# Kernel optimization log

Hardware: AMD Instinct MI355X
Metric: run time of the kernel (lower is better)

The kernel has to match this reference:

```python
import jax, jax.numpy as jnp
import numpy as np
from jax import lax

# Parameter physical bounds, order: smax, k1, k2, kb
MIN_BOUNDS = np.array([10.0, 0.01, 0.001, 0.001], dtype=np.float32)
MAX_BOUNDS = np.array([500.0, 0.9, 0.2, 0.1], dtype=np.float32)

T, B, H = 2048, 32, 64
N_FORCING, N_STATE, N_PARAM, N_FLUX = 2, 2, 4, 4


def setup_inputs() -> dict:
    key = jax.random.key(0)
    k1, k2 = jax.random.split(key)
    # forcings: [T, B, H, 2] -> (P precip, PET potential ET), non-negative
    forcings = jax.random.uniform(k1, (T, B, H, N_FORCING), dtype=jnp.float32)
    # initial states: [B, H, 2], model default is zeros
    states = jnp.zeros((B, H, N_STATE), dtype=jnp.float32)
    # unconstrained params in [0,1): [B, H, 4] (static -> repeated over T)
    parameters = jax.random.uniform(k2, (B, H, N_PARAM), dtype=jnp.float32)
    return {"forcings": forcings, "states": states, "parameters": parameters}


def _core(states_t, forcings_t, params_t):
    # states_t: [B,H,2], forcings_t: [B,H,2], params_t: [B,H,4]
    S1, S2 = states_t[..., 0], states_t[..., 1]
    P, PET = forcings_t[..., 0], forcings_t[..., 1]
    smax, k1, k2, kb = (params_t[..., i] for i in range(4))
    # flux_calculator
    et = PET * jnp.clip(S1 / smax, 0.0, 1.0)
    q1 = k1 * S1
    perc = k2 * S1
    qb = kb * S2
    fluxes = jnp.stack([et, q1, perc, qb], axis=-1)  # [B,H,4]
    # state_updater (mass balance), then clamp_(min=0)
    S1n = S1 + P - et - q1 - perc
    S2n = S2 + perc - qb
    new_states = jnp.maximum(jnp.stack([S1n, S2n], axis=-1), 0.0)  # [B,H,2]
    return fluxes, new_states


def reference(forcings, states, parameters):
    # transform parameters to physical bounds: min + (max-min)*u
    min_b = jnp.asarray(MIN_BOUNDS)
    max_b = jnp.asarray(MAX_BOUNDS)
    phys_params = min_b + (max_b - min_b) * parameters  # [B,H,4] (static)

    def step(carry, f_t):
        fluxes_t, new_states = _core(carry, f_t, phys_params)
        return new_states, (fluxes_t, new_states)

    _, (fluxes_seq, states_seq) = lax.scan(step, states, forcings)
    # fluxes_seq: [T,B,H,4], states_seq: [T,B,H,2]
    return fluxes_seq, states_seq
```

## Files before the change

kernel.cpp:

```cpp
#include <hip/hip_runtime.h>
#include <stdint.h>

#define T_STEPS 2048
#define N_CELLS 2048
#define GCELLS  64
#define NGROUPS (N_CELLS / GCELLS)
#define TS      128
#define NTILES  (T_STEPS / TS)
#define BCHUNK  16
#define NCHUNK  (T_STEPS / BCHUNK)
#define FLUX_ELEMS ((size_t)T_STEPS * N_CELLS * 4)

#define AS3 __attribute__((address_space(3)))
#define AS1 __attribute__((address_space(1)))

__device__ __forceinline__ void step_state(float& S1, float& S2,
                                           float P, float PET,
                                           float inv_smax, float a, float b,
                                           float k2) {
    float ratio = fminf(S1 * inv_smax, 1.0f);
    float u1    = fmaf(S1, a, P);
    float S1n   = fmaxf(fmaf(-PET, ratio, u1), 0.0f);
    float perc  = k2 * S1;
    float S2n   = fmaxf(fmaf(S2, b, perc), 0.0f);
    S1 = S1n; S2 = S2n;
}

__global__ void __launch_bounds__(64) hydro_scan(
    const float* __restrict__ forc,
    const float* __restrict__ init_state,
    const float* __restrict__ params,
    float* __restrict__ out)
{
    __shared__ float4 tile[2][TS * 32];

    const int g    = blockIdx.x;
    const int L    = threadIdx.x;
    const int cell = g * GCELLS + L;

    float2* out_s = (float2*)(out + FLUX_ELEMS);

    const float4* gf4 = (const float4*)forc;
    const size_t lane_off = (size_t)(L >> 5) * 1024 + (size_t)g * 32 + (L & 31);

    const float4 u = ((const float4*)params)[cell];
    float2 s0 = ((const float2*)init_state)[cell];

    {
        const float4* gp = gf4 + lane_off;
        AS3 char* lp = (AS3 char*)(void*)tile[0];
        #pragma unroll
        for (int k = 0; k < 64; ++k)
            __builtin_amdgcn_global_load_lds((AS1 const void*)(gp + (size_t)k * 2048),
                                             (AS3 void*)(lp + (size_t)k * 1024),
                                             16, 0, 0);
    }

    const float smax = 10.0f  + 490.0f * u.x;
    const float k1   = 0.01f  + 0.89f  * u.y;
    const float k2   = 0.001f + 0.199f * u.z;
    const float kb   = 0.001f + 0.099f * u.w;
    const float inv_smax = 1.0f / smax;
    const float a = 1.0f - k1 - k2;
    const float b = 1.0f - kb;
    float S1 = s0.x, S2 = s0.y;

    asm volatile("s_waitcnt vmcnt(0)" ::: "memory");

    for (int s = 0; s < NTILES; ++s) {
        if (s + 1 < NTILES) {
            const float4* gp = gf4 + (size_t)(s + 1) * TS * 1024 + lane_off;
            AS3 char* lp = (AS3 char*)(void*)tile[(s + 1) & 1];
            #pragma unroll
            for (int k = 0; k < 64; ++k)
                __builtin_amdgcn_global_load_lds((AS1 const void*)(gp + (size_t)k * 2048),
                                                 (AS3 void*)(lp + (size_t)k * 1024),
                                                 16, 0, 0);
        }

        const float2* tp = (const float2*)tile[s & 1];
        float2 buf[2][8];
        #pragma unroll
        for (int j = 0; j < 8; ++j) buf[0][j] = tp[j * GCELLS + L];

        #pragma unroll
        for (int grp = 0; grp < TS / 8; ++grp) {
            const int cur = grp & 1, nxt = cur ^ 1;
            if (grp < TS / 8 - 1) {
                #pragma unroll
                for (int j = 0; j < 8; ++j)
                    buf[nxt][j] = tp[((grp + 1) * 8 + j) * GCELLS + L];
            }
            #pragma unroll
            for (int j = 0; j < 8; ++j)
                step_state(S1, S2, buf[cur][j].x, buf[cur][j].y,
                           inv_smax, a, b, k2);
            if ((grp & 1) == 1 && !(s == NTILES - 1 && grp == TS / 8 - 1)) {
                int t = s * TS + grp * 8 + 7;
                out_s[(size_t)t * N_CELLS + cell] = make_float2(S1, S2);
            }
        }

        asm volatile("s_waitcnt vmcnt(0)" ::: "memory");
    }
}

__global__ void __launch_bounds__(256) hydro_expand(
    const float* __restrict__ forc,
    const float* __restrict__ init_state,
    const float* __restrict__ params,
    float* __restrict__ out)
{
    const int blk  = blockIdx.x;
    const int wave = threadIdx.x >> 6;
    const int L    = threadIdx.x & 63;
    const int c    = blk >> 3;
    const int g    = (blk & 7) * 4 + wave;
    const int cell = g * GCELLS + L;
    const int t0   = c * BCHUNK;

    float4* out_f = (float4*)out;
    float2* out_s = (float2*)(out + FLUX_ELEMS);
    const float2* fp = (const float2*)forc;
    size_t idx = (size_t)t0 * N_CELLS + cell;

    float2 fb[BCHUNK];
    #pragma unroll
    for (int j = 0; j < BCHUNK; ++j) fb[j] = fp[idx + (size_t)j * N_CELLS];

    const float4 u = ((const float4*)params)[cell];
    float2 sp = (c == 0) ? ((const float2*)init_state)[cell]
                         : out_s[(size_t)(t0 - 1) * N_CELLS + cell];

    const float smax = 10.0f  + 490.0f * u.x;
    const float k1   = 0.01f  + 0.89f  * u.y;
    const float k2   = 0.001f + 0.199f * u.z;
    const float kb   = 0.001f + 0.099f * u.w;
    const float inv_smax = 1.0f / smax;
    const float a = 1.0f - k1 - k2;
    const float b = 1.0f - kb;
    float S1 = sp.x, S2 = sp.y;

    #pragma unroll
    for (int j = 0; j < BCHUNK; ++j) {
        float P = fb[j].x, PET = fb[j].y;
        float ratio = fminf(S1 * inv_smax, 1.0f);
        float et    = PET * ratio;
        float q1    = k1 * S1;
        float perc  = k2 * S1;
        float qb    = kb * S2;
        float u1  = fmaf(S1, a, P);
        float S1n = fmaxf(fmaf(-PET, ratio, u1), 0.0f);
        float S2n = fmaxf(fmaf(S2, b, perc), 0.0f);
        size_t o = idx + (size_t)j * N_CELLS;
        out_f[o] = make_float4(et, q1, perc, qb);
        out_s[o] = make_float2(S1n, S2n);
        S1 = S1n; S2 = S2n;
    }
}

extern "C" void kernel_launch(void* const* d_in, const int* in_sizes, int n_in,
                              void* d_out, int out_size, void* d_ws, size_t ws_size,
                              hipStream_t stream) {
    const float* forc = (const float*)d_in[0];
    const float* st0  = (const float*)d_in[1];
    const float* prm  = (const float*)d_in[2];
    float* out  = (float*)d_out;

    hipLaunchKernelGGL(hydro_scan, dim3(NGROUPS), dim3(GCELLS), 0, stream,
                       forc, st0, prm, out);
    hipLaunchKernelGGL(hydro_expand, dim3(NCHUNK * NGROUPS / 4), dim3(256), 0, stream,
                       forc, st0, prm, out);
}
```

Before: 186.7 us.

## Shorten scan recurrence chain and deepen forcing prefetch ring to four buffers

```diff
diff --git a/kernel.cpp b/kernel.cpp
--- a/kernel.cpp
+++ b/kernel.cpp
@@ -5,8 +5,8 @@
 #define N_CELLS 2048
 #define GCELLS  64
 #define NGROUPS (N_CELLS / GCELLS)
-#define TS      128
-#define NTILES  (T_STEPS / TS)
+#define CH      32
+#define NCH     (T_STEPS / CH)
 #define BCHUNK  16
 #define NCHUNK  (T_STEPS / BCHUNK)
 #define FLUX_ELEMS ((size_t)T_STEPS * N_CELLS * 4)
@@ -18,12 +18,14 @@
                                            float P, float PET,
                                            float inv_smax, float a, float b,
                                            float k2) {
-    float ratio = fminf(S1 * inv_smax, 1.0f);
-    float u1    = fmaf(S1, a, P);
-    float S1n   = fmaxf(fmaf(-PET, ratio, u1), 0.0f);
-    float perc  = k2 * S1;
-    float S2n   = fmaxf(fmaf(S2, b, perc), 0.0f);
-    S1 = S1n; S2 = S2n;
+    float a_c  = fmaf(-PET, inv_smax, a);
+    float PmP  = P - PET;
+    float t1   = fmaf(S1, a_c, P);
+    float t2   = fmaf(S1, a, PmP);
+    float S1n  = fmaxf(fmaxf(t1, t2), 0.0f);
+    float perc = k2 * S1;
+    S2 = fmaf(S2, b, perc);
+    S1 = S1n;
 }
 
 __global__ void __launch_bounds__(64) hydro_scan(
@@ -32,7 +34,7 @@
     const float* __restrict__ params,
     float* __restrict__ out)
 {
-    __shared__ float4 tile[2][TS * 32];
+    __shared__ float4 tile[4][CH * 32];
 
     const int g    = blockIdx.x;
     const int L    = threadIdx.x;
@@ -43,18 +45,20 @@
     const float4* gf4 = (const float4*)forc;
     const size_t lane_off = (size_t)(L >> 5) * 1024 + (size_t)g * 32 + (L & 31);
 
+#define ISSUE_DMA(c_) do {                                                     \
+        const float4* gp_ = gf4 + (size_t)(c_) * (CH * 1024) + lane_off;       \
+        AS3 char* lp_ = (AS3 char*)(void*)tile[(c_) & 3];                      \
+        _Pragma("unroll")                                                      \
+        for (int k_ = 0; k_ < 16; ++k_)                                        \
+            __builtin_amdgcn_global_load_lds(                                  \
+                (AS1 const void*)(gp_ + (size_t)k_ * 2048),                    \
+                (AS3 void*)(lp_ + (size_t)k_ * 1024), 16, 0, 0);               \
+    } while (0)
+
     const float4 u = ((const float4*)params)[cell];
     float2 s0 = ((const float2*)init_state)[cell];
 
-    {
-        const float4* gp = gf4 + lane_off;
-        AS3 char* lp = (AS3 char*)(void*)tile[0];
-        #pragma unroll
-        for (int k = 0; k < 64; ++k)
-            __builtin_amdgcn_global_load_lds((AS1 const void*)(gp + (size_t)k * 2048),
-                                             (AS3 void*)(lp + (size_t)k * 1024),
-                                             16, 0, 0);
-    }
+    ISSUE_DMA(0); ISSUE_DMA(1); ISSUE_DMA(2);
 
     const float smax = 10.0f  + 490.0f * u.x;
     const float k1   = 0.01f  + 0.89f  * u.y;
@@ -65,44 +69,57 @@
     const float b = 1.0f - kb;
     float S1 = s0.x, S2 = s0.y;
 
-    asm volatile("s_waitcnt vmcnt(0)" ::: "memory");
+    asm volatile("s_waitcnt vmcnt(32)" ::: "memory");
+    __builtin_amdgcn_sched_barrier(0);
 
-    for (int s = 0; s < NTILES; ++s) {
-        if (s + 1 < NTILES) {
-            const float4* gp = gf4 + (size_t)(s + 1) * TS * 1024 + lane_off;
-            AS3 char* lp = (AS3 char*)(void*)tile[(s + 1) & 1];
-            #pragma unroll
-            for (int k = 0; k < 64; ++k)
-                __builtin_amdgcn_global_load_lds((AS1 const void*)(gp + (size_t)k * 2048),
-                                                 (AS3 void*)(lp + (size_t)k * 1024),
-                                                 16, 0, 0);
-        }
+    float2 buf[2][8];
+    {
+        const float2* tp0 = (const float2*)tile[0];
+        #pragma unroll
+        for (int j = 0; j < 8; ++j) buf[0][j] = tp0[j * GCELLS + L];
+    }
 
-        const float2* tp = (const float2*)tile[s & 1];
-        float2 buf[2][8];
-        #pragma unroll
-        for (int j = 0; j < 8; ++j) buf[0][j] = tp[j * GCELLS + L];
+    for (int c = 0; c < NCH; ++c) {
+        const float2* tp  = (const float2*)tile[c & 3];
+        const float2* tpn = (const float2*)tile[(c + 1) & 3];
 
         #pragma unroll
-        for (int grp = 0; grp < TS / 8; ++grp) {
+        for (int grp = 0; grp < 4; ++grp) {
             const int cur = grp & 1, nxt = cur ^ 1;
-            if (grp < TS / 8 - 1) {
+
+            if (grp < 3) {
                 #pragma unroll
                 for (int j = 0; j < 8; ++j)
                     buf[nxt][j] = tp[((grp + 1) * 8 + j) * GCELLS + L];
+            } else {
+                if (c <= NCH - 4) {
+                    ISSUE_DMA(c + 3);
+                    asm volatile("s_waitcnt vmcnt(32)" ::: "memory");
+                } else if (c == NCH - 3) {
+                    asm volatile("s_waitcnt vmcnt(16)" ::: "memory");
+                } else if (c == NCH - 2) {
+                    asm volatile("s_waitcnt vmcnt(0)" ::: "memory");
+                }
+                __builtin_amdgcn_sched_barrier(0);
+                if (c < NCH - 1) {
+                    #pragma unroll
+                    for (int j = 0; j < 8; ++j)
+                        buf[nxt][j] = tpn[j * GCELLS + L];
+                }
             }
+
             #pragma unroll
             for (int j = 0; j < 8; ++j)
                 step_state(S1, S2, buf[cur][j].x, buf[cur][j].y,
                            inv_smax, a, b, k2);
-            if ((grp & 1) == 1 && !(s == NTILES - 1 && grp == TS / 8 - 1)) {
-                int t = s * TS + grp * 8 + 7;
+
+            if ((grp & 1) == 1 && !(c == NCH - 1 && grp == 3)) {
+                int t = c * CH + grp * 8 + 7;
                 out_s[(size_t)t * N_CELLS + cell] = make_float2(S1, S2);
             }
         }
-
-        asm volatile("s_waitcnt vmcnt(0)" ::: "memory");
     }
+#undef ISSUE_DMA
 }
 
 __global__ void __launch_bounds__(256) hydro_expand(
@@ -149,13 +166,12 @@
         float q1    = k1 * S1;
         float perc  = k2 * S1;
         float qb    = kb * S2;
-        float u1  = fmaf(S1, a, P);
-        float S1n = fmaxf(fmaf(-PET, ratio, u1), 0.0f);
-        float S2n = fmaxf(fmaf(S2, b, perc), 0.0f);
+        float S1s = S1, S2s = S2;
+        step_state(S1s, S2s, P, PET, inv_smax, a, b, k2);
         size_t o = idx + (size_t)j * N_CELLS;
         out_f[o] = make_float4(et, q1, perc, qb);
-        out_s[o] = make_float2(S1n, S2n);
-        S1 = S1n; S2 = S2n;
+        out_s[o] = make_float2(S1s, S2s);
+        S1 = S1s; S2 = S2s;
     }
 }
 
```

New measurement: 191.8 us. 1.03x slower.
